# Kernel optimization log

Measured on AMD Instinct MI355X. Metric: run time of the kernel, lower is better.

## Reference

```python
import jax, jax.numpy as jnp
import numpy as np

N_NODES = 100000
N_EDGES = 1600000
D_FEAT = 64      # per-node embedding dim; nin = 2*D_FEAT = 128
N_OUT = 64
NSLOPE = 0.2


def setup_inputs() -> dict:
    key = jax.random.key(0)
    k0, k1, k2, k3, k4, k5 = jax.random.split(key, 6)
    nodes = jax.random.normal(k0, (N_NODES, D_FEAT), dtype=jnp.float32)
    src = jax.random.randint(k1, (N_EDGES,), 0, N_NODES, dtype=jnp.int32)
    dst = jax.random.randint(k2, (N_EDGES,), 0, N_NODES, dtype=jnp.int32)
    # Linear(nin=2*D_FEAT, nout=N_OUT) weight/bias and Linear(nout,1,bias=False)
    W_w = jax.random.normal(k3, (N_OUT, 2 * D_FEAT), dtype=jnp.float32) * (2 * D_FEAT) ** -0.5
    W_b = jax.random.normal(k4, (N_OUT,), dtype=jnp.float32) * 0.02
    a_w = jax.random.normal(k5, (N_OUT,), dtype=jnp.float32) * N_OUT ** -0.5
    return {"nodes": nodes, "src": src, "dst": dst, "W_w": W_w, "W_b": W_b, "a_w": a_w}


def reference(nodes, src, dst, W_w, W_b, a_w):
    # Per edge: score = a( LeakyReLU( W [h_src ; h_dst] + b ) )
    # Split W over the concat so we project each node once, then gather.
    d = nodes.shape[1]
    W1, W2 = W_w[:, :d], W_w[:, d:]          # [nout, d] each
    p1 = nodes @ W1.T                        # [N, nout]
    p2 = nodes @ W2.T                        # [N, nout]
    hw = p1[src] + p2[dst] + W_b             # [E, nout]  (== W(cat(hi,hj)))
    act = jnp.where(hw >= 0, hw, NSLOPE * hw)  # LeakyReLU
    scores = act @ a_w                       # [E]
    # Sparse softmax over dim=1 of the [N,N] score matrix == segment softmax
    # over edges grouped by the row (src) index, numerically stabilized.
    n = nodes.shape[0]
    m = jax.ops.segment_max(scores, src, num_segments=n)   # [N]
    e = jnp.exp(scores - m[src])                            # [E]
    s = jax.ops.segment_sum(e, src, num_segments=n)         # [N]
    attn = e / s[src]                                       # [E]
    return attn
```

## Files before the change

### kernel.cpp

```cpp
#include <hip/hip_runtime.h>

#define NSLOPE 0.2f

typedef __attribute__((ext_vector_type(8))) short short8;
typedef __attribute__((ext_vector_type(4))) float floatx4;

static __device__ inline unsigned short f2bf(float f) {
    unsigned u = __float_as_uint(f);
    unsigned r = u + 0x7FFFu + ((u >> 16) & 1u);
    return (unsigned short)(r >> 16);
}
static __device__ inline float bflo(unsigned u) { return __uint_as_float(u << 16); }
static __device__ inline float bfhi(unsigned u) { return __uint_as_float(u & 0xFFFF0000u); }

#define PNB 128
#define AST 72

__global__ __launch_bounds__(256) void proj_mfma_kernel(
    const float* __restrict__ nodes, const float* __restrict__ Ww,
    const float* __restrict__ Wb,
    unsigned short* __restrict__ P1, unsigned short* __restrict__ P2,
    float* __restrict__ ssum, int nNodes)
{
    __shared__ unsigned short aT[PNB * AST];
    __shared__ unsigned short wT[128 * AST];
    const int t = threadIdx.x;
    const int base = blockIdx.x * PNB;

    if (t < PNB) { int n = base + t; if (n < nNodes) ssum[n] = 0.f; }

    for (int f = t; f < PNB * 16; f += 256) {
        int n = f >> 4, dpos = (f & 15) * 4;
        float4 v = make_float4(0.f, 0.f, 0.f, 0.f);
        if (base + n < nNodes) v = *(const float4*)(nodes + (size_t)(base + n) * 64 + dpos);
        ushort4 o;
        o.x = f2bf(v.x); o.y = f2bf(v.y); o.z = f2bf(v.z); o.w = f2bf(v.w);
        *(ushort4*)&aT[n * AST + dpos] = o;
    }
    for (int i = t; i < 2048; i += 256) {
        float4 v = *(const float4*)(Ww + i * 4);
        int o = i >> 5;
        int c = (i * 4) & 127;
        int j, k;
        if (c < 64) { j = o;      k = c;      }
        else        { j = 64 + o; k = c - 64; }
        ushort4 w4;
        w4.x = f2bf(v.x); w4.y = f2bf(v.y); w4.z = f2bf(v.z); w4.w = f2bf(v.w);
        *(ushort4*)&wT[j * AST + k] = w4;
    }
    __syncthreads();

    const int w = t >> 6, lane = t & 63;
    const int lr = lane & 15;
    const int lk = (lane >> 4) * 8;

    floatx4 acc[2][8];
    #pragma unroll
    for (int rt = 0; rt < 2; rt++)
        #pragma unroll
        for (int ct = 0; ct < 8; ct++) acc[rt][ct] = (floatx4){0.f, 0.f, 0.f, 0.f};

    #pragma unroll
    for (int ks = 0; ks < 2; ks++) {
        int k0 = ks * 32 + lk;
        short8 a0 = *(const short8*)&aT[((w * 2 + 0) * 16 + lr) * AST + k0];
        short8 a1 = *(const short8*)&aT[((w * 2 + 1) * 16 + lr) * AST + k0];
        #pragma unroll
        for (int ct = 0; ct < 8; ct++) {
            short8 b = *(const short8*)&wT[(ct * 16 + lr) * AST + k0];
            acc[0][ct] = __builtin_amdgcn_mfma_f32_16x16x32_bf16(a0, b, acc[0][ct], 0, 0, 0);
            acc[1][ct] = __builtin_amdgcn_mfma_f32_16x16x32_bf16(a1, b, acc[1][ct], 0, 0, 0);
        }
    }

    #pragma unroll
    for (int ct = 0; ct < 8; ct++) {
        int j = ct * 16 + lr;
        float bias = (j < 64) ? Wb[j] : 0.f;
        #pragma unroll
        for (int rt = 0; rt < 2; rt++) {
            #pragma unroll
            for (int r = 0; r < 4; r++) {
                int nl = (w * 2 + rt) * 16 + (lane >> 4) * 4 + r;
                int n = base + nl;
                if (n < nNodes) {
                    unsigned short val = f2bf(acc[rt][ct][r] + bias);
                    if (j < 64) P1[(size_t)n * 64 + j]      = val;
                    else        P2[(size_t)n * 64 + j - 64] = val;
                }
            }
        }
    }
}

__global__ __launch_bounds__(256) void edge_score_kernel(
    const unsigned short* __restrict__ P1, const unsigned short* __restrict__ P2,
    const int* __restrict__ src, const int* __restrict__ dst,
    const float* __restrict__ a_w,
    float* __restrict__ evals, float* __restrict__ ssum, int nE)
{
    int tid = blockIdx.x * 256 + threadIdx.x;
    int e   = tid >> 3;
    int sub = tid & 7;
    if (e >= nE) return;

    int s = src[e];
    int d = dst[e];
    uint4 r1 = *(const uint4*)(P1 + (size_t)s * 64 + sub * 8);
    uint4 r2 = *(const uint4*)(P2 + (size_t)d * 64 + sub * 8);
    float4 a0 = *(const float4*)(a_w + sub * 8);
    float4 a1 = *(const float4*)(a_w + sub * 8 + 4);

    float partial = 0.f, h;
    h = bflo(r1.x) + bflo(r2.x); h = (h >= 0.f) ? h : NSLOPE * h; partial = fmaf(h, a0.x, partial);
    h = bfhi(r1.x) + bfhi(r2.x); h = (h >= 0.f) ? h : NSLOPE * h; partial = fmaf(h, a0.y, partial);
    h = bflo(r1.y) + bflo(r2.y); h = (h >= 0.f) ? h : NSLOPE * h; partial = fmaf(h, a0.z, partial);
    h = bfhi(r1.y) + bfhi(r2.y); h = (h >= 0.f) ? h : NSLOPE * h; partial = fmaf(h, a0.w, partial);
    h = bflo(r1.z) + bflo(r2.z); h = (h >= 0.f) ? h : NSLOPE * h; partial = fmaf(h, a1.x, partial);
    h = bfhi(r1.z) + bfhi(r2.z); h = (h >= 0.f) ? h : NSLOPE * h; partial = fmaf(h, a1.y, partial);
    h = bflo(r1.w) + bflo(r2.w); h = (h >= 0.f) ? h : NSLOPE * h; partial = fmaf(h, a1.z, partial);
    h = bfhi(r1.w) + bfhi(r2.w); h = (h >= 0.f) ? h : NSLOPE * h; partial = fmaf(h, a1.w, partial);

    partial += __shfl_xor(partial, 1);
    partial += __shfl_xor(partial, 2);
    partial += __shfl_xor(partial, 4);

    if (sub == 0) {
        float ev = __expf(partial);
        evals[e] = ev;
        atomicAdd(&ssum[s], ev);
    }
}

__global__ __launch_bounds__(256) void normalize_kernel(
    const int* __restrict__ src, const float* __restrict__ ssum,
    float* __restrict__ out, int nE)
{
    int i = blockIdx.x * 256 + threadIdx.x;
    int e4 = i * 4;
    if (e4 + 3 < nE) {
        float4 ev = *(const float4*)(out + e4);
        int4   sv = *(const int4*)(src + e4);
        float4 r;
        r.x = ev.x / ssum[sv.x];
        r.y = ev.y / ssum[sv.y];
        r.z = ev.z / ssum[sv.z];
        r.w = ev.w / ssum[sv.w];
        *(float4*)(out + e4) = r;
    } else {
        for (int e = e4; e < nE; ++e) out[e] = out[e] / ssum[src[e]];
    }
}

extern "C" void kernel_launch(void* const* d_in, const int* in_sizes, int n_in,
                              void* d_out, int out_size, void* d_ws, size_t ws_size,
                              hipStream_t stream) {
    (void)n_in; (void)out_size; (void)ws_size;
    const float* nodes = (const float*)d_in[0];
    const int*   src   = (const int*)d_in[1];
    const int*   dst   = (const int*)d_in[2];
    const float* Ww    = (const float*)d_in[3];
    const float* Wb    = (const float*)d_in[4];
    const float* a_w   = (const float*)d_in[5];
    float* out = (float*)d_out;

    const int nNodes = in_sizes[0] / 64;
    const int nE     = in_sizes[1];

    unsigned short* P1   = (unsigned short*)d_ws;
    unsigned short* P2   = P1 + (size_t)nNodes * 64;
    float*          ssum = (float*)(P2 + (size_t)nNodes * 64);

    int nblocks_proj = (nNodes + PNB - 1) / PNB;
    proj_mfma_kernel<<<nblocks_proj, 256, 0, stream>>>(nodes, Ww, Wb, P1, P2, ssum, nNodes);

    int nblocks_edge = (int)(((long long)nE * 8 + 255) / 256);
    edge_score_kernel<<<nblocks_edge, 256, 0, stream>>>(P1, P2, src, dst, a_w, out, ssum, nE);

    int nthreads_norm = (nE + 3) / 4;
    int nblocks_norm  = (nthreads_norm + 255) / 256;
    normalize_kernel<<<nblocks_norm, 256, 0, stream>>>(src, ssum, out, nE);
}
```

Baseline: 125.7 us.

## Use persistent grid-stride edge kernel with software-prefetched gathers

The edge-score kernel now launches a fixed grid of 2048 blocks. Each group of 8 threads loops over edges in a grid stride, loading the next edge's src/dst indices and P1/P2 rows before computing the current edge's score. The a_w weights are hoisted out of the loop. The aim is to overlap the dependent random gathers with compute and cut block launch overhead, at the cost of more registers and a fixed grid size that may underfill or overfill the device.

```diff
diff --git a/kernel.cpp b/kernel.cpp
--- a/kernel.cpp
+++ b/kernel.cpp
@@ -93,42 +93,59 @@
     }
 }
 
-__global__ __launch_bounds__(256) void edge_score_kernel(
+__global__ __launch_bounds__(256, 8) void edge_score_kernel(
     const unsigned short* __restrict__ P1, const unsigned short* __restrict__ P2,
     const int* __restrict__ src, const int* __restrict__ dst,
     const float* __restrict__ a_w,
     float* __restrict__ evals, float* __restrict__ ssum, int nE)
 {
-    int tid = blockIdx.x * 256 + threadIdx.x;
-    int e   = tid >> 3;
-    int sub = tid & 7;
+    const int sub = threadIdx.x & 7;
+    const int g0  = blockIdx.x * 32 + (threadIdx.x >> 3);
+    const int G   = gridDim.x * 32;
+
+    const float4 a0 = *(const float4*)(a_w + sub * 8);
+    const float4 a1 = *(const float4*)(a_w + sub * 8 + 4);
+
+    int e = g0;
     if (e >= nE) return;
 
-    int s = src[e];
-    int d = dst[e];
-    uint4 r1 = *(const uint4*)(P1 + (size_t)s * 64 + sub * 8);
-    uint4 r2 = *(const uint4*)(P2 + (size_t)d * 64 + sub * 8);
-    float4 a0 = *(const float4*)(a_w + sub * 8);
-    float4 a1 = *(const float4*)(a_w + sub * 8 + 4);
+    int sCur = src[e];
+    int dCur = dst[e];
+    uint4 A = *(const uint4*)(P1 + (size_t)sCur * 64 + sub * 8);
+    uint4 B = *(const uint4*)(P2 + (size_t)dCur * 64 + sub * 8);
 
-    float partial = 0.f, h;
-    h = bflo(r1.x) + bflo(r2.x); h = (h >= 0.f) ? h : NSLOPE * h; partial = fmaf(h, a0.x, partial);
-    h = bfhi(r1.x) + bfhi(r2.x); h = (h >= 0.f) ? h : NSLOPE * h; partial = fmaf(h, a0.y, partial);
-    h = bflo(r1.y) + bflo(r2.y); h = (h >= 0.f) ? h : NSLOPE * h; partial = fmaf(h, a0.z, partial);
-    h = bfhi(r1.y) + bfhi(r2.y); h = (h >= 0.f) ? h : NSLOPE * h; partial = fmaf(h, a0.w, partial);
-    h = bflo(r1.z) + bflo(r2.z); h = (h >= 0.f) ? h : NSLOPE * h; partial = fmaf(h, a1.x, partial);
-    h = bfhi(r1.z) + bfhi(r2.z); h = (h >= 0.f) ? h : NSLOPE * h; partial = fmaf(h, a1.y, partial);
-    h = bflo(r1.w) + bflo(r2.w); h = (h >= 0.f) ? h : NSLOPE * h; partial = fmaf(h, a1.z, partial);
-    h = bfhi(r1.w) + bfhi(r2.w); h = (h >= 0.f) ? h : NSLOPE * h; partial = fmaf(h, a1.w, partial);
+    while (e < nE) {
+        const int e2 = e + G;
+        int s2 = 0;
+        uint4 A2, B2;
+        if (e2 < nE) {
+            s2 = src[e2];
+            int d2 = dst[e2];
+            A2 = *(const uint4*)(P1 + (size_t)s2 * 64 + sub * 8);
+            B2 = *(const uint4*)(P2 + (size_t)d2 * 64 + sub * 8);
+        }
 
-    partial += __shfl_xor(partial, 1);
-    partial += __shfl_xor(partial, 2);
-    partial += __shfl_xor(partial, 4);
+        float p = 0.f, h;
+        h = bflo(A.x) + bflo(B.x); h = (h >= 0.f) ? h : NSLOPE * h; p = fmaf(h, a0.x, p);
+        h = bfhi(A.x) + bfhi(B.x); h = (h >= 0.f) ? h : NSLOPE * h; p = fmaf(h, a0.y, p);
+        h = bflo(A.y) + bflo(B.y); h = (h >= 0.f) ? h : NSLOPE * h; p = fmaf(h, a0.z, p);
+        h = bfhi(A.y) + bfhi(B.y); h = (h >= 0.f) ? h : NSLOPE * h; p = fmaf(h, a0.w, p);
+        h = bflo(A.z) + bflo(B.z); h = (h >= 0.f) ? h : NSLOPE * h; p = fmaf(h, a1.x, p);
+        h = bfhi(A.z) + bfhi(B.z); h = (h >= 0.f) ? h : NSLOPE * h; p = fmaf(h, a1.y, p);
+        h = bflo(A.w) + bflo(B.w); h = (h >= 0.f) ? h : NSLOPE * h; p = fmaf(h, a1.z, p);
+        h = bfhi(A.w) + bfhi(B.w); h = (h >= 0.f) ? h : NSLOPE * h; p = fmaf(h, a1.w, p);
 
-    if (sub == 0) {
-        float ev = __expf(partial);
-        evals[e] = ev;
-        atomicAdd(&ssum[s], ev);
+        p += __shfl_xor(p, 1);
+        p += __shfl_xor(p, 2);
+        p += __shfl_xor(p, 4);
+
+        if (sub == 0) {
+            float ev = __expf(p);
+            evals[e] = ev;
+            atomicAdd(&ssum[sCur], ev);
+        }
+
+        e = e2; sCur = s2; A = A2; B = B2;
     }
 }
 
@@ -174,8 +191,7 @@
     int nblocks_proj = (nNodes + PNB - 1) / PNB;
     proj_mfma_kernel<<<nblocks_proj, 256, 0, stream>>>(nodes, Ww, Wb, P1, P2, ssum, nNodes);
 
-    int nblocks_edge = (int)(((long long)nE * 8 + 255) / 256);
-    edge_score_kernel<<<nblocks_edge, 256, 0, stream>>>(P1, P2, src, dst, a_w, out, ssum, nE);
+    edge_score_kernel<<<2048, 256, 0, stream>>>(P1, P2, src, dst, a_w, out, ssum, nE);
 
     int nthreads_norm = (nE + 3) / 4;
     int nblocks_norm  = (nthreads_norm + 255) / 256;
```

Measured after the change: 130.4 us. 3.8% more time.
